# Kernel tuning notes

Measured on AMD Instinct MI355X. Metric: run time of the kernel, lower is better.

The kernel has to match this reference:

```python
import jax, jax.numpy as jnp
import numpy as np

N_NODES = 100000
N_EDGES = 1600000
D_IN = 64
D_HID = 64


def setup_inputs() -> dict:
    key = jax.random.key(0)
    k_x, k_e, k_wl, k_wr, k_b = jax.random.split(key, 5)
    x = jax.random.normal(k_x, (N_NODES, D_IN), dtype=jnp.float32)
    edge_index = jax.random.randint(k_e, (2, N_EDGES), 0, N_NODES, dtype=jnp.int64)
    # SAGEConv params: lin_l (applied to aggregated neighbors, has bias),
    # lin_r (applied to root/self, no bias). Stored as [in, out] for x @ W.
    scale = 1.0 / np.sqrt(D_IN)
    W_l = jax.random.uniform(k_wl, (D_IN, D_HID), jnp.float32, -scale, scale)
    W_r = jax.random.uniform(k_wr, (D_IN, D_HID), jnp.float32, -scale, scale)
    b = jax.random.uniform(k_b, (D_HID,), jnp.float32, -scale, scale)
    return {"x": x, "edge_index": edge_index, "W_l": W_l, "W_r": W_r, "b": b}


def reference(x, edge_index, W_l, W_r, b):
    # GraphSAGE 1-layer: mean-aggregate neighbor feats, linear, add root term, ReLU.
    src = edge_index[0]  # message sources (neighbors j)
    dst = edge_index[1]  # message targets (nodes i)
    n = x.shape[0]
    msg = x[src]  # [E, D_IN] irregular gather
    s = jax.ops.segment_sum(msg, dst, num_segments=n)  # [N, D_IN]
    cnt = jax.ops.segment_sum(jnp.ones((src.shape[0],), x.dtype), dst, num_segments=n)
    agg = s / jnp.maximum(cnt, 1.0)[:, None]  # mean aggregation
    out = agg @ W_l + x @ W_r + b  # SAGEConv: lin_l(agg) + lin_r(x)
    return jax.nn.relu(out)
```

## Files before the change

### kernel.cpp

```cpp
#include <hip/hip_runtime.h>
#include <hip/hip_bf16.h>

#define D 64
#define CHUNK 4096
#define NBKT_SHIFT 7
#define NSUB 8
#define SUBCAP 720
#define CAPN 45
#define CAPB (CAPN * 128)
#define PAD 16

__global__ __launch_bounds__(256) void k_scatter(
        const int* __restrict__ src, const int* __restrict__ dst,
        int* __restrict__ cursor, int* __restrict__ pairs,
        int nE, int nB) {
    __shared__ int hA[800], bL[800], hC[800];
    const int t = threadIdx.x;
    const int bid = blockIdx.x;
    const int e0 = bid * CHUNK;
    const int cnt = min(CHUNK, nE - e0);
    const int sub = bid & (NSUB - 1);

    int rd[16], rs[16];
#pragma unroll
    for (int j = 0; j < 16; ++j) {
        int i = t + j * 256;
        rd[j] = (i < cnt) ? dst[e0 + i] : -1;
    }
#pragma unroll
    for (int j = 0; j < 16; ++j) {
        int i = t + j * 256;
        rs[j] = (i < cnt) ? src[e0 + i] : 0;
    }

    for (int i = t; i < nB; i += 256) { hA[i] = 0; hC[i] = 0; }
    __syncthreads();
#pragma unroll
    for (int j = 0; j < 16; ++j)
        if (rd[j] >= 0) atomicAdd(&hA[rd[j] >> NBKT_SHIFT], 1);
    __syncthreads();
    const int start = (bid * 401) % nB;
    for (int i = t; i < nB; i += 256) {
        int bk = i + start; if (bk >= nB) bk -= nB;
        int c = hA[bk];
        bL[bk] = (c > 0) ? atomicAdd(&cursor[(bk * NSUB + sub) * PAD], c) : 0;
    }
    __syncthreads();
#pragma unroll
    for (int j = 0; j < 16; ++j) {
        int d = rd[j];
        if (d < 0) continue;
        int bk = d >> NBKT_SHIFT;
        int r = atomicAdd(&hC[bk], 1);
        int p = bL[bk] + r;
        if (p < SUBCAP)
            pairs[(size_t)bk * CAPB + sub * SUBCAP + p] = ((d & 127) << 17) | rs[j];
    }
}

__global__ __launch_bounds__(256) void k_pre(
        const float* __restrict__ x, const float* __restrict__ Wl,
        const float* __restrict__ Wr, const float* __restrict__ b,
        unsigned short* __restrict__ ylb, float* __restrict__ out, int nN) {
    __shared__ float sXT[64 * 65];
    __shared__ float4 sW4[2048];
    __shared__ float sB[64];

    const int t = threadIdx.x;
    const int tile = blockIdx.x * 64;

    {
        const float4* wl4p = (const float4*)Wl;
        const float4* wr4p = (const float4*)Wr;
#pragma unroll
        for (int i = 0; i < 4; ++i) {
            int idx = t + i * 256;
            sW4[idx] = wl4p[idx];
            sW4[1024 + idx] = wr4p[idx];
        }
    }
    if (t < 64) sB[t] = b[t];
#pragma unroll
    for (int i = 0; i < 4; ++i) {
        int idx = t + i * 256;
        int row = idx >> 4;
        int col4 = (idx & 15) * 4;
        int gg = tile + row;
        float4 v = (gg < nN) ? *(const float4*)&x[(size_t)gg * D + col4]
                             : make_float4(0.f, 0.f, 0.f, 0.f);
        sXT[(col4 + 0) * 65 + row] = v.x;
        sXT[(col4 + 1) * 65 + row] = v.y;
        sXT[(col4 + 2) * 65 + row] = v.z;
        sXT[(col4 + 3) * 65 + row] = v.w;
    }
    __syncthreads();

    const int n0 = (t & 15) * 4;
    const int c0v = t >> 4;
    float accl[4][4] = {}, accr[4][4] = {};
#pragma unroll 4
    for (int k = 0; k < D; ++k) {
        float4 a4  = *(const float4*)&sXT[k * 65 + n0];
        float4 wl4 = sW4[k * 16 + c0v];
        float4 wr4 = sW4[1024 + k * 16 + c0v];
        accl[0][0] += a4.x * wl4.x; accl[0][1] += a4.x * wl4.y; accl[0][2] += a4.x * wl4.z; accl[0][3] += a4.x * wl4.w;
        accl[1][0] += a4.y * wl4.x; accl[1][1] += a4.y * wl4.y; accl[1][2] += a4.y * wl4.z; accl[1][3] += a4.y * wl4.w;
        accl[2][0] += a4.z * wl4.x; accl[2][1] += a4.z * wl4.y; accl[2][2] += a4.z * wl4.z; accl[2][3] += a4.z * wl4.w;
        accl[3][0] += a4.w * wl4.x; accl[3][1] += a4.w * wl4.y; accl[3][2] += a4.w * wl4.z; accl[3][3] += a4.w * wl4.w;
        accr[0][0] += a4.x * wr4.x; accr[0][1] += a4.x * wr4.y; accr[0][2] += a4.x * wr4.z; accr[0][3] += a4.x * wr4.w;
        accr[1][0] += a4.y * wr4.x; accr[1][1] += a4.y * wr4.y; accr[1][2] += a4.y * wr4.z; accr[1][3] += a4.y * wr4.w;
        accr[2][0] += a4.z * wr4.x; accr[2][1] += a4.z * wr4.y; accr[2][2] += a4.z * wr4.z; accr[2][3] += a4.z * wr4.w;
        accr[3][0] += a4.w * wr4.x; accr[3][1] += a4.w * wr4.y; accr[3][2] += a4.w * wr4.z; accr[3][3] += a4.w * wr4.w;
    }

    const int c0 = c0v * 4;
#pragma unroll
    for (int i = 0; i < 4; ++i) {
        int gg = tile + n0 + i;
        if (gg >= nN) continue;
        __hip_bfloat162 l01 = __float22bfloat162_rn(make_float2(accl[i][0], accl[i][1]));
        __hip_bfloat162 l23 = __float22bfloat162_rn(make_float2(accl[i][2], accl[i][3]));
        uint2 pl = make_uint2(*(unsigned int*)&l01, *(unsigned int*)&l23);
        *(uint2*)&ylb[(size_t)gg * D + c0] = pl;
        float4 o;
        o.x = accr[i][0] + sB[c0 + 0];
        o.y = accr[i][1] + sB[c0 + 1];
        o.z = accr[i][2] + sB[c0 + 2];
        o.w = accr[i][3] + sB[c0 + 3];
        *(float4*)&out[(size_t)gg * D + c0] = o;
    }
}

__global__ __launch_bounds__(256) void k_sort(
        int* __restrict__ pairs, const int* __restrict__ cursor,
        int* __restrict__ cnt, int nN, int nB) {
    __shared__ int h[128];
    const int bkt = blockIdx.x;
    const int t = threadIdx.x;
    const size_t base = (size_t)bkt * CAPB;

    if (t < 128) h[t] = 0;

    int st[24];
#pragma unroll
    for (int j = 0; j < NSUB; ++j) {
        int c = min(cursor[(bkt * NSUB + j) * PAD], SUBCAP);
#pragma unroll
        for (int w = 0; w < 3; ++w) {
            int i = t + w * 256;
            st[j * 3 + w] = (i < c) ? pairs[base + j * SUBCAP + i] : -1;
        }
    }
    __syncthreads();

#pragma unroll
    for (int j = 0; j < 24; ++j) {
        int v = st[j];
        if (v >= 0) {
            int dl = v >> 17;
            int r = atomicAdd(&h[dl], 1);
            if (r < CAPN) pairs[base + dl * CAPN + r] = v & 0x1FFFF;
        }
    }
    __syncthreads();

    if (t < 128) {
        int nd = bkt * 128 + t;
        if (nd < nN) cnt[nd] = h[t];
    }
}

__device__ __forceinline__ float bl(unsigned p) { return __uint_as_float(p << 16); }
__device__ __forceinline__ float bh(unsigned p) { return __uint_as_float(p & 0xffff0000u); }

__global__ __launch_bounds__(256) void k_gather(
        const unsigned int* __restrict__ ylb, const int* __restrict__ cnt,
        const int* __restrict__ slots, float* __restrict__ out, int nN, int cap) {
    const int t = threadIdx.x;
    const int lane32 = t & 31;
    const int node = blockIdx.x * 8 + (t >> 5);
    if (node >= nN) return;

    const int deg = cnt[node];
    const int n = min(deg, cap);
    const size_t base = (size_t)node * cap;

    int idxA = (lane32 < n) ? slots[base + lane32] : 0;
    int idxB = (32 + lane32 < n) ? slots[base + 32 + lane32] : 0;

    float s0 = 0.f, s1 = 0.f, t0 = 0.f, t1 = 0.f;
    float u0 = 0.f, u1 = 0.f, v0 = 0.f, v1 = 0.f;

    const int n1 = min(n, 32);
    int k = 0;
    for (; k + 4 <= n1; k += 4) {
        int i0 = __shfl(idxA, k, 32), i1 = __shfl(idxA, k + 1, 32);
        int i2 = __shfl(idxA, k + 2, 32), i3 = __shfl(idxA, k + 3, 32);
        unsigned p0 = ylb[(size_t)i0 * 32 + lane32];
        unsigned p1 = ylb[(size_t)i1 * 32 + lane32];
        unsigned p2 = ylb[(size_t)i2 * 32 + lane32];
        unsigned p3 = ylb[(size_t)i3 * 32 + lane32];
        s0 += bl(p0); s1 += bh(p0);
        t0 += bl(p1); t1 += bh(p1);
        u0 += bl(p2); u1 += bh(p2);
        v0 += bl(p3); v1 += bh(p3);
    }
    for (; k < n1; ++k) {
        int i0 = __shfl(idxA, k, 32);
        unsigned p0 = ylb[(size_t)i0 * 32 + lane32];
        s0 += bl(p0); s1 += bh(p0);
    }
    const int n2 = n - 32;
    k = 0;
    for (; k + 4 <= n2; k += 4) {
        int i0 = __shfl(idxB, k, 32), i1 = __shfl(idxB, k + 1, 32);
        int i2 = __shfl(idxB, k + 2, 32), i3 = __shfl(idxB, k + 3, 32);
        unsigned p0 = ylb[(size_t)i0 * 32 + lane32];
        unsigned p1 = ylb[(size_t)i1 * 32 + lane32];
        unsigned p2 = ylb[(size_t)i2 * 32 + lane32];
        unsigned p3 = ylb[(size_t)i3 * 32 + lane32];
        s0 += bl(p0); s1 += bh(p0);
        t0 += bl(p1); t1 += bh(p1);
        u0 += bl(p2); u1 += bh(p2);
        v0 += bl(p3); v1 += bh(p3);
    }
    for (; k < n2; ++k) {
        int i0 = __shfl(idxB, k, 32);
        unsigned p0 = ylb[(size_t)i0 * 32 + lane32];
        s0 += bl(p0); s1 += bh(p0);
    }

    const float inv = 1.f / fmaxf((float)deg, 1.f);
    const float m0 = ((s0 + t0) + (u0 + v0)) * inv;
    const float m1 = ((s1 + t1) + (u1 + v1)) * inv;

    float2* po = (float2*)&out[(size_t)node * D + lane32 * 2];
    float2 rr = *po;
    rr.x = fmaxf(m0 + rr.x, 0.f);
    rr.y = fmaxf(m1 + rr.y, 0.f);
    *po = rr;
}

extern "C" void kernel_launch(void* const* d_in, const int* in_sizes, int n_in,
                              void* d_out, int out_size, void* d_ws, size_t ws_size,
                              hipStream_t stream) {
    const float* x  = (const float*)d_in[0];
    const int*   ei = (const int*)d_in[1];
    const float* Wl = (const float*)d_in[2];
    const float* Wr = (const float*)d_in[3];
    const float* b  = (const float*)d_in[4];
    float*       out = (float*)d_out;

    const int nN = in_sizes[0] / D;
    const int nE = in_sizes[1] / 2;
    const int* src = ei;
    const int* dst = ei + nE;

    const int nB = (nN + 127) >> NBKT_SHIFT;

    int* cursor = (int*)d_ws;
    int* pairs  = cursor + (size_t)nB * NSUB * PAD;
    int* cnt    = pairs + (size_t)nB * CAPB;
    size_t off = (size_t)nB * NSUB * PAD + (size_t)nB * CAPB + (size_t)nN;
    off = (off + 3) & ~(size_t)3;
    unsigned short* ylb = (unsigned short*)((int*)d_ws + off);

    hipMemsetAsync(cursor, 0, (size_t)nB * NSUB * PAD * sizeof(int), stream);

    k_scatter<<<(nE + CHUNK - 1) / CHUNK, 256, 0, stream>>>(src, dst, cursor, pairs, nE, nB);
    k_pre<<<(nN + 63) / 64, 256, 0, stream>>>(x, Wl, Wr, b, ylb, out, nN);
    k_sort<<<nB, 256, 0, stream>>>(pairs, cursor, cnt, nN, nB);
    k_gather<<<(nN + 7) / 8, 256, 0, stream>>>((const unsigned int*)ylb, cnt,
                                               pairs, out, nN, CAPN);
}
```

Before: 182.9 us.

## Merge scatter and projection into one interleaved launch; widen gather loads to 8 bytes

The edge-bucketing scatter and the per-node projection kernels are combined into a single launch. Blocks are interleaved proportionally so that scatter blocks and dense projection blocks run concurrently, and one kernel launch and its tail are removed. The gather kernel now uses 16 lanes per node with 64-bit loads of four bf16 values each, so each lane issues half as many load instructions and each block covers more nodes. The trade-offs are a larger shared-memory union per block, which may lower occupancy for the scatter blocks, and a third index register because the gather now uses 16-wide shuffles.

```diff
diff --git a/kernel.cpp b/kernel.cpp
--- a/kernel.cpp
+++ b/kernel.cpp
@@ -10,64 +10,73 @@
 #define CAPB (CAPN * 128)
 #define PAD 16
 
-__global__ __launch_bounds__(256) void k_scatter(
-        const int* __restrict__ src, const int* __restrict__ dst,
+__global__ __launch_bounds__(256) void k_combo(
+        const float* __restrict__ x, const int* __restrict__ src,
+        const int* __restrict__ dst, const float* __restrict__ Wl,
+        const float* __restrict__ Wr, const float* __restrict__ b,
         int* __restrict__ cursor, int* __restrict__ pairs,
-        int nE, int nB) {
-    __shared__ int hA[800], bL[800], hC[800];
+        unsigned short* __restrict__ ylb, float* __restrict__ out,
+        int nE, int nN, int nB, int nA, int total) {
+    __shared__ __align__(16) char smem[49664];
+
+    const int bid = blockIdx.x;
     const int t = threadIdx.x;
-    const int bid = blockIdx.x;
-    const int e0 = bid * CHUNK;
-    const int cnt = min(CHUNK, nE - e0);
-    const int sub = bid & (NSUB - 1);
-
-    int rd[16], rs[16];
-#pragma unroll
-    for (int j = 0; j < 16; ++j) {
-        int i = t + j * 256;
-        rd[j] = (i < cnt) ? dst[e0 + i] : -1;
-    }
-#pragma unroll
-    for (int j = 0; j < 16; ++j) {
-        int i = t + j * 256;
-        rs[j] = (i < cnt) ? src[e0 + i] : 0;
-    }
-
-    for (int i = t; i < nB; i += 256) { hA[i] = 0; hC[i] = 0; }
-    __syncthreads();
-#pragma unroll
-    for (int j = 0; j < 16; ++j)
-        if (rd[j] >= 0) atomicAdd(&hA[rd[j] >> NBKT_SHIFT], 1);
-    __syncthreads();
-    const int start = (bid * 401) % nB;
-    for (int i = t; i < nB; i += 256) {
-        int bk = i + start; if (bk >= nB) bk -= nB;
-        int c = hA[bk];
-        bL[bk] = (c > 0) ? atomicAdd(&cursor[(bk * NSUB + sub) * PAD], c) : 0;
-    }
-    __syncthreads();
-#pragma unroll
-    for (int j = 0; j < 16; ++j) {
-        int d = rd[j];
-        if (d < 0) continue;
-        int bk = d >> NBKT_SHIFT;
-        int r = atomicAdd(&hC[bk], 1);
-        int p = bL[bk] + r;
-        if (p < SUBCAP)
-            pairs[(size_t)bk * CAPB + sub * SUBCAP + p] = ((d & 127) << 17) | rs[j];
-    }
-}
-
-__global__ __launch_bounds__(256) void k_pre(
-        const float* __restrict__ x, const float* __restrict__ Wl,
-        const float* __restrict__ Wr, const float* __restrict__ b,
-        unsigned short* __restrict__ ylb, float* __restrict__ out, int nN) {
-    __shared__ float sXT[64 * 65];
-    __shared__ float4 sW4[2048];
-    __shared__ float sB[64];
-
-    const int t = threadIdx.x;
-    const int tile = blockIdx.x * 64;
+
+    const long long lo = ((long long)bid * nA) / total;
+    const long long hi = ((long long)(bid + 1) * nA) / total;
+
+    if (hi > lo) {
+        int* hA = (int*)smem;
+        int* bL = hA + 800;
+        int* hC = bL + 800;
+        const int chunk = (int)lo;
+        const int e0 = chunk * CHUNK;
+        const int cnt = min(CHUNK, nE - e0);
+        const int sub = chunk & (NSUB - 1);
+
+        int rd[16], rs[16];
+#pragma unroll
+        for (int j = 0; j < 16; ++j) {
+            int i = t + j * 256;
+            rd[j] = (i < cnt) ? dst[e0 + i] : -1;
+        }
+#pragma unroll
+        for (int j = 0; j < 16; ++j) {
+            int i = t + j * 256;
+            rs[j] = (i < cnt) ? src[e0 + i] : 0;
+        }
+
+        for (int i = t; i < nB; i += 256) { hA[i] = 0; hC[i] = 0; }
+        __syncthreads();
+#pragma unroll
+        for (int j = 0; j < 16; ++j)
+            if (rd[j] >= 0) atomicAdd(&hA[rd[j] >> NBKT_SHIFT], 1);
+        __syncthreads();
+        const int start = (chunk * 401) % nB;
+        for (int i = t; i < nB; i += 256) {
+            int bk = i + start; if (bk >= nB) bk -= nB;
+            int c = hA[bk];
+            bL[bk] = (c > 0) ? atomicAdd(&cursor[(bk * NSUB + sub) * PAD], c) : 0;
+        }
+        __syncthreads();
+#pragma unroll
+        for (int j = 0; j < 16; ++j) {
+            int d = rd[j];
+            if (d < 0) continue;
+            int bk = d >> NBKT_SHIFT;
+            int r = atomicAdd(&hC[bk], 1);
+            int p = bL[bk] + r;
+            if (p < SUBCAP)
+                pairs[(size_t)bk * CAPB + sub * SUBCAP + p] = ((d & 127) << 17) | rs[j];
+        }
+        return;
+    }
+
+    const int g = bid - (int)lo;
+    float*  sXT = (float*)smem;
+    float4* sW4 = (float4*)(smem + 16640);
+    float*  sB  = (float*)(smem + 16640 + 32768);
+    const int tile = g * 64;
 
     {
         const float4* wl4p = (const float4*)Wl;
@@ -170,74 +179,93 @@
     }
 }
 
-__device__ __forceinline__ float bl(unsigned p) { return __uint_as_float(p << 16); }
-__device__ __forceinline__ float bh(unsigned p) { return __uint_as_float(p & 0xffff0000u); }
+#define ACC4(p, q0, q1, q2, q3)                                   \
+    {                                                             \
+        unsigned lo32 = (unsigned)(p), hi32 = (unsigned)((p) >> 32); \
+        q0 += __uint_as_float(lo32 << 16);                        \
+        q1 += __uint_as_float(lo32 & 0xffff0000u);                \
+        q2 += __uint_as_float(hi32 << 16);                        \
+        q3 += __uint_as_float(hi32 & 0xffff0000u);                \
+    }
 
 __global__ __launch_bounds__(256) void k_gather(
-        const unsigned int* __restrict__ ylb, const int* __restrict__ cnt,
+        const unsigned long long* __restrict__ ylb8, const int* __restrict__ cnt,
         const int* __restrict__ slots, float* __restrict__ out, int nN, int cap) {
     const int t = threadIdx.x;
-    const int lane32 = t & 31;
-    const int node = blockIdx.x * 8 + (t >> 5);
+    const int l = t & 15;
+    const int node = blockIdx.x * 16 + (t >> 4);
     if (node >= nN) return;
 
     const int deg = cnt[node];
     const int n = min(deg, cap);
     const size_t base = (size_t)node * cap;
 
-    int idxA = (lane32 < n) ? slots[base + lane32] : 0;
-    int idxB = (32 + lane32 < n) ? slots[base + 32 + lane32] : 0;
-
-    float s0 = 0.f, s1 = 0.f, t0 = 0.f, t1 = 0.f;
-    float u0 = 0.f, u1 = 0.f, v0 = 0.f, v1 = 0.f;
-
-    const int n1 = min(n, 32);
+    int idxA = (l < n) ? slots[base + l] : 0;
+    int idxB = (16 + l < n) ? slots[base + 16 + l] : 0;
+    int idxC = (32 + l < n) ? slots[base + 32 + l] : 0;
+
+    float qa0 = 0.f, qa1 = 0.f, qa2 = 0.f, qa3 = 0.f;
+    float qb0 = 0.f, qb1 = 0.f, qb2 = 0.f, qb3 = 0.f;
+
+    const int n1 = min(n, 16);
     int k = 0;
     for (; k + 4 <= n1; k += 4) {
-        int i0 = __shfl(idxA, k, 32), i1 = __shfl(idxA, k + 1, 32);
-        int i2 = __shfl(idxA, k + 2, 32), i3 = __shfl(idxA, k + 3, 32);
-        unsigned p0 = ylb[(size_t)i0 * 32 + lane32];
-        unsigned p1 = ylb[(size_t)i1 * 32 + lane32];
-        unsigned p2 = ylb[(size_t)i2 * 32 + lane32];
-        unsigned p3 = ylb[(size_t)i3 * 32 + lane32];
-        s0 += bl(p0); s1 += bh(p0);
-        t0 += bl(p1); t1 += bh(p1);
-        u0 += bl(p2); u1 += bh(p2);
-        v0 += bl(p3); v1 += bh(p3);
+        int i0 = __shfl(idxA, k, 16), i1 = __shfl(idxA, k + 1, 16);
+        int i2 = __shfl(idxA, k + 2, 16), i3 = __shfl(idxA, k + 3, 16);
+        unsigned long long p0 = ylb8[(size_t)i0 * 16 + l];
+        unsigned long long p1 = ylb8[(size_t)i1 * 16 + l];
+        unsigned long long p2 = ylb8[(size_t)i2 * 16 + l];
+        unsigned long long p3 = ylb8[(size_t)i3 * 16 + l];
+        ACC4(p0, qa0, qa1, qa2, qa3); ACC4(p1, qb0, qb1, qb2, qb3);
+        ACC4(p2, qa0, qa1, qa2, qa3); ACC4(p3, qb0, qb1, qb2, qb3);
     }
     for (; k < n1; ++k) {
-        int i0 = __shfl(idxA, k, 32);
-        unsigned p0 = ylb[(size_t)i0 * 32 + lane32];
-        s0 += bl(p0); s1 += bh(p0);
-    }
-    const int n2 = n - 32;
+        int i0 = __shfl(idxA, k, 16);
+        unsigned long long p0 = ylb8[(size_t)i0 * 16 + l];
+        ACC4(p0, qa0, qa1, qa2, qa3);
+    }
+    const int n2 = min(n, 32) - 16;
     k = 0;
     for (; k + 4 <= n2; k += 4) {
-        int i0 = __shfl(idxB, k, 32), i1 = __shfl(idxB, k + 1, 32);
-        int i2 = __shfl(idxB, k + 2, 32), i3 = __shfl(idxB, k + 3, 32);
-        unsigned p0 = ylb[(size_t)i0 * 32 + lane32];
-        unsigned p1 = ylb[(size_t)i1 * 32 + lane32];
-        unsigned p2 = ylb[(size_t)i2 * 32 + lane32];
-        unsigned p3 = ylb[(size_t)i3 * 32 + lane32];
-        s0 += bl(p0); s1 += bh(p0);
-        t0 += bl(p1); t1 += bh(p1);
-        u0 += bl(p2); u1 += bh(p2);
-        v0 += bl(p3); v1 += bh(p3);
+        int i0 = __shfl(idxB, k, 16), i1 = __shfl(idxB, k + 1, 16);
+        int i2 = __shfl(idxB, k + 2, 16), i3 = __shfl(idxB, k + 3, 16);
+        unsigned long long p0 = ylb8[(size_t)i0 * 16 + l];
+        unsigned long long p1 = ylb8[(size_t)i1 * 16 + l];
+        unsigned long long p2 = ylb8[(size_t)i2 * 16 + l];
+        unsigned long long p3 = ylb8[(size_t)i3 * 16 + l];
+        ACC4(p0, qa0, qa1, qa2, qa3); ACC4(p1, qb0, qb1, qb2, qb3);
+        ACC4(p2, qa0, qa1, qa2, qa3); ACC4(p3, qb0, qb1, qb2, qb3);
     }
     for (; k < n2; ++k) {
-        int i0 = __shfl(idxB, k, 32);
-        unsigned p0 = ylb[(size_t)i0 * 32 + lane32];
-        s0 += bl(p0); s1 += bh(p0);
+        int i0 = __shfl(idxB, k, 16);
+        unsigned long long p0 = ylb8[(size_t)i0 * 16 + l];
+        ACC4(p0, qa0, qa1, qa2, qa3);
+    }
+    const int n3 = n - 32;
+    k = 0;
+    for (; k + 4 <= n3; k += 4) {
+        int i0 = __shfl(idxC, k, 16), i1 = __shfl(idxC, k + 1, 16);
+        int i2 = __shfl(idxC, k + 2, 16), i3 = __shfl(idxC, k + 3, 16);
+        unsigned long long p0 = ylb8[(size_t)i0 * 16 + l];
+        unsigned long long p1 = ylb8[(size_t)i1 * 16 + l];
+        unsigned long long p2 = ylb8[(size_t)i2 * 16 + l];
+        unsigned long long p3 = ylb8[(size_t)i3 * 16 + l];
+        ACC4(p0, qa0, qa1, qa2, qa3); ACC4(p1, qb0, qb1, qb2, qb3);
+        ACC4(p2, qa0, qa1, qa2, qa3); ACC4(p3, qb0, qb1, qb2, qb3);
+    }
+    for (; k < n3; ++k) {
+        int i0 = __shfl(idxC, k, 16);
+        unsigned long long p0 = ylb8[(size_t)i0 * 16 + l];
+        ACC4(p0, qa0, qa1, qa2, qa3);
     }
 
     const float inv = 1.f / fmaxf((float)deg, 1.f);
-    const float m0 = ((s0 + t0) + (u0 + v0)) * inv;
-    const float m1 = ((s1 + t1) + (u1 + v1)) * inv;
-
-    float2* po = (float2*)&out[(size_t)node * D + lane32 * 2];
-    float2 rr = *po;
-    rr.x = fmaxf(m0 + rr.x, 0.f);
-    rr.y = fmaxf(m1 + rr.y, 0.f);
+    float4* po = (float4*)&out[(size_t)node * D + l * 4];
+    float4 rr = *po;
+    rr.x = fmaxf((qa0 + qb0) * inv + rr.x, 0.f);
+    rr.y = fmaxf((qa1 + qb1) * inv + rr.y, 0.f);
+    rr.z = fmaxf((qa2 + qb2) * inv + rr.z, 0.f);
+    rr.w = fmaxf((qa3 + qb3) * inv + rr.w, 0.f);
     *po = rr;
 }
 
@@ -267,9 +295,13 @@
 
     hipMemsetAsync(cursor, 0, (size_t)nB * NSUB * PAD * sizeof(int), stream);
 
-    k_scatter<<<(nE + CHUNK - 1) / CHUNK, 256, 0, stream>>>(src, dst, cursor, pairs, nE, nB);
-    k_pre<<<(nN + 63) / 64, 256, 0, stream>>>(x, Wl, Wr, b, ylb, out, nN);
+    const int nA    = (nE + CHUNK - 1) / CHUNK;
+    const int nPre  = (nN + 63) / 64;
+    const int total = nA + nPre;
+
+    k_combo<<<total, 256, 0, stream>>>(x, src, dst, Wl, Wr, b,
+                                       cursor, pairs, ylb, out, nE, nN, nB, nA, total);
     k_sort<<<nB, 256, 0, stream>>>(pairs, cursor, cnt, nN, nB);
-    k_gather<<<(nN + 7) / 8, 256, 0, stream>>>((const unsigned int*)ylb, cnt,
-                                               pairs, out, nN, CAPN);
+    k_gather<<<(nN + 15) / 16, 256, 0, stream>>>((const unsigned long long*)ylb,
+                                                 cnt, pairs, out, nN, CAPN);
 }
```

New measurement: 186.0 us. Within noise of the previous version (+1.7%).
